# Kernel optimization log

Measured on AMD Instinct MI355X. Metric: run time of the kernel, lower is better.

Reference implementation:

```python
import jax, jax.numpy as jnp
import numpy as np

N_MQ = 50000   # number of 'mq' (user/query) nodes
N_SQ = 50000   # number of 'sq' (movie/sub-query) nodes
E = 600000     # edges of type ('mq','queries','sq'); reverse edges are the flip
EL = 200000    # supervision edges for the classifier
H = 128        # hidden_channels
F_IN = 768     # raw 'sq' feature dim (movie_lin in_features)
N_LAYERS = 4


def setup_inputs() -> dict:
    key = jax.random.key(0)
    ks = jax.random.split(key, 12)
    sH = 1.0 / np.sqrt(H)
    sF = 1.0 / np.sqrt(F_IN)
    return {
        "mq_node_id": jnp.arange(N_MQ, dtype=jnp.int64) if jax.config.jax_enable_x64 else jnp.arange(N_MQ, dtype=jnp.int32),
        "sq_node_id": jnp.arange(N_SQ, dtype=jnp.int32),
        "sq_x": jax.random.normal(ks[0], (N_SQ, F_IN), jnp.float32),
        "edge_index": jax.random.randint(ks[1], (2, E), 0, N_SQ),
        "edge_label_index": jax.random.randint(ks[2], (2, EL), 0, N_SQ),
        "user_emb": jax.random.normal(ks[3], (N_MQ, H), jnp.float32) * 0.1,
        "movie_emb": jax.random.normal(ks[4], (N_SQ, H), jnp.float32) * 0.1,
        "lin_W": jax.random.normal(ks[5], (H, F_IN), jnp.float32) * sF,
        "lin_b": jnp.zeros((H,), jnp.float32),
        "Wl_s": jax.random.normal(ks[6], (N_LAYERS, H, H), jnp.float32) * sH,
        "bl_s": jnp.zeros((N_LAYERS, H), jnp.float32),
        "Wr_s": jax.random.normal(ks[7], (N_LAYERS, H, H), jnp.float32) * sH,
        "Wl_m": jax.random.normal(ks[8], (N_LAYERS, H, H), jnp.float32) * sH,
        "bl_m": jnp.zeros((N_LAYERS, H), jnp.float32),
        "Wr_m": jax.random.normal(ks[9], (N_LAYERS, H, H), jnp.float32) * sH,
    }


def _sage(x_src, x_dst, src_idx, dst_idx, Wl, bl, Wr, n_dst):
    """PyG SAGEConv (aggr='mean', root_weight=True, bias on lin_l only)."""
    msg = x_src[src_idx]                                     # [E, H] gather
    agg = jax.ops.segment_sum(msg, dst_idx, num_segments=n_dst)
    cnt = jax.ops.segment_sum(jnp.ones((src_idx.shape[0], 1), x_src.dtype),
                              dst_idx, num_segments=n_dst)
    mean = agg / jnp.maximum(cnt, 1.0)                       # mean over in-neighbors
    return mean @ Wl.T + bl + x_dst @ Wr.T


def reference(mq_node_id, sq_node_id, sq_x, edge_index, edge_label_index,
              user_emb, movie_emb, lin_W, lin_b,
              Wl_s, bl_s, Wr_s, Wl_m, bl_m, Wr_m):
    # input encoders
    x_mq = user_emb[mq_node_id]                              # [N_MQ, H]
    x_sq = sq_x @ lin_W.T + lin_b + movie_emb[sq_node_id]    # [N_SQ, H]
    src, dst = edge_index[0], edge_index[1]                  # mq -> sq; reverse is flip
    for i in range(N_LAYERS):
        new_sq = _sage(x_mq, x_sq, src, dst, Wl_s[i], bl_s[i], Wr_s[i], N_SQ)
        new_mq = _sage(x_sq, x_mq, dst, src, Wl_m[i], bl_m[i], Wr_m[i], N_MQ)
        if i == 0:  # only conv1 has ReLU in the original GNN
            new_sq = jax.nn.relu(new_sq)
            new_mq = jax.nn.relu(new_mq)
        x_mq, x_sq = new_mq, new_sq
    # dot-product classifier over supervision edges
    return (x_mq[edge_label_index[0]] * x_sq[edge_label_index[1]]).sum(axis=-1)
```

## Files before the change

### kernel.cpp

```cpp
#include <hip/hip_runtime.h>

#define H    128
#define NMQ  50000
#define NSQ  50000
#define NE   600000
#define NEL  200000
#define FIN  768
#define NLAYERS 4

typedef __attribute__((ext_vector_type(8))) short bf16x8;
typedef __attribute__((ext_vector_type(4))) float f32x4;

__device__ inline ushort f2b(float f) {
  unsigned u = __float_as_uint(f);
  u = (u + 0x7FFFu + ((u >> 16) & 1u)) >> 16;
  return (ushort)u;
}
__device__ inline float b2f(ushort h) { return __uint_as_float((unsigned)h << 16); }

__global__ void cvt_bf16(const float* __restrict__ in, ushort* __restrict__ out, int n4) {
  int i = blockIdx.x * blockDim.x + threadIdx.x;
  if (i >= n4) return;
  float4 v = ((const float4*)in)[i];
  ushort4 o;
  o.x = f2b(v.x); o.y = f2b(v.y); o.z = f2b(v.z); o.w = f2b(v.w);
  ((ushort4*)out)[i] = o;
}

__global__ __launch_bounds__(64) void encoder_mfma(
    const float* __restrict__ A, const ushort* __restrict__ Wb,
    const float* __restrict__ bias, const float* __restrict__ memb,
    ushort* __restrict__ C)
{
  int lane = threadIdx.x;
  int rowbase = blockIdx.x * 16;
  int t = lane >> 4, fr = lane & 15;
  f32x4 acc[8];
  #pragma unroll
  for (int c = 0; c < 8; ++c)
    #pragma unroll
    for (int q = 0; q < 4; ++q) acc[c][q] = 0.f;

  int arow = rowbase + fr;
  const float* Abase = A + (long)arow * FIN + t * 8;

  for (int k0 = 0; k0 < FIN; k0 += 32) {
    bf16x8 af, bfm[8];
    {
      const float* p = Abase + k0;
      float4 v0 = *(const float4*)p;
      float4 v1 = *(const float4*)(p + 4);
      ushort tmp[8];
      tmp[0] = f2b(v0.x); tmp[1] = f2b(v0.y); tmp[2] = f2b(v0.z); tmp[3] = f2b(v0.w);
      tmp[4] = f2b(v1.x); tmp[5] = f2b(v1.y); tmp[6] = f2b(v1.z); tmp[7] = f2b(v1.w);
      af = *(bf16x8*)tmp;
    }
    #pragma unroll
    for (int cc = 0; cc < 8; ++cc) {
      int col = cc * 16 + fr;
      bfm[cc] = *(const bf16x8*)(Wb + (long)col * FIN + k0 + t * 8);
    }
    #pragma unroll
    for (int cc = 0; cc < 8; ++cc)
      acc[cc] = __builtin_amdgcn_mfma_f32_16x16x32_bf16(af, bfm[cc], acc[cc], 0, 0, 0);
  }
  #pragma unroll
  for (int cc = 0; cc < 8; ++cc)
    #pragma unroll
    for (int q = 0; q < 4; ++q) {
      int row = rowbase + t * 4 + q;
      int col = cc * 16 + fr;
      float v = acc[cc][q] + bias[col] + memb[(long)row * H + col];
      C[(long)row * H + col] = f2b(v);
    }
}

__global__ __launch_bounds__(64) void fused_layer(
    const ushort* __restrict__ xg,
    const ushort* __restrict__ xs,
    const int* __restrict__ offs, const int* __restrict__ csr,
    const ushort* __restrict__ Wl, const ushort* __restrict__ Wr,
    const float* __restrict__ bias,
    ushort* __restrict__ Cout, int M, int relu)
{
  __shared__ ushort mtile[16 * 128];
  int lane = threadIdx.x;
  int rowbase = blockIdx.x * 16;
  const unsigned* X = (const unsigned*)xg;

  int wslot = lane >> 2;
  unsigned* mt32 = (unsigned*)mtile;
  for (int i = 0; i < 16; ++i) {
    int row = rowbase + i;
    int s = offs[row], e = offs[row + 1];
    float a0 = 0.f, a1 = 0.f;
    int j = s;
    for (; j + 8 <= e; j += 8) {
      long i0 = csr[j], i1 = csr[j+1], i2 = csr[j+2], i3 = csr[j+3];
      long i4 = csr[j+4], i5 = csr[j+5], i6 = csr[j+6], i7 = csr[j+7];
      unsigned x0 = X[i0*64+lane], x1 = X[i1*64+lane], x2 = X[i2*64+lane], x3 = X[i3*64+lane];
      unsigned x4 = X[i4*64+lane], x5 = X[i5*64+lane], x6 = X[i6*64+lane], x7 = X[i7*64+lane];
      a0 += b2f((ushort)(x0 & 0xffff)) + b2f((ushort)(x1 & 0xffff))
          + b2f((ushort)(x2 & 0xffff)) + b2f((ushort)(x3 & 0xffff))
          + b2f((ushort)(x4 & 0xffff)) + b2f((ushort)(x5 & 0xffff))
          + b2f((ushort)(x6 & 0xffff)) + b2f((ushort)(x7 & 0xffff));
      a1 += b2f((ushort)(x0 >> 16)) + b2f((ushort)(x1 >> 16))
          + b2f((ushort)(x2 >> 16)) + b2f((ushort)(x3 >> 16))
          + b2f((ushort)(x4 >> 16)) + b2f((ushort)(x5 >> 16))
          + b2f((ushort)(x6 >> 16)) + b2f((ushort)(x7 >> 16));
    }
    if (j + 4 <= e) {
      long i0 = csr[j], i1 = csr[j+1], i2 = csr[j+2], i3 = csr[j+3];
      unsigned x0 = X[i0*64+lane], x1 = X[i1*64+lane], x2 = X[i2*64+lane], x3 = X[i3*64+lane];
      a0 += b2f((ushort)(x0 & 0xffff)) + b2f((ushort)(x1 & 0xffff))
          + b2f((ushort)(x2 & 0xffff)) + b2f((ushort)(x3 & 0xffff));
      a1 += b2f((ushort)(x0 >> 16)) + b2f((ushort)(x1 >> 16))
          + b2f((ushort)(x2 >> 16)) + b2f((ushort)(x3 >> 16));
      j += 4;
    }
    for (; j < e; ++j) {
      unsigned x = X[(long)csr[j] * 64 + lane];
      a0 += b2f((ushort)(x & 0xffff));
      a1 += b2f((ushort)(x >> 16));
    }
    float inv = (e > s) ? 1.f / (float)(e - s) : 0.f;
    a0 *= inv; a1 *= inv;
    int sw = (wslot & 8) | ((wslot & 7) ^ (i & 7));
    mt32[i * 64 + sw * 4 + (lane & 3)] = (unsigned)f2b(a0) | ((unsigned)f2b(a1) << 16);
  }

  int t = lane >> 4, fr = lane & 15;
  f32x4 acc[8];
  #pragma unroll
  for (int c = 0; c < 8; ++c)
    #pragma unroll
    for (int q = 0; q < 4; ++q) acc[c][q] = 0.f;

  #pragma unroll
  for (int ks = 0; ks < 4; ++ks) {
    int slot = ks * 4 + t;
    int sw = (slot & 8) | ((slot & 7) ^ (fr & 7));
    bf16x8 af = *(const bf16x8*)&mtile[fr * 128 + sw * 8];
    bf16x8 bfm[8];
    #pragma unroll
    for (int cc = 0; cc < 8; ++cc) {
      int col = cc * 16 + fr;
      bfm[cc] = *(const bf16x8*)(Wl + (long)col * H + slot * 8);
    }
    #pragma unroll
    for (int cc = 0; cc < 8; ++cc)
      acc[cc] = __builtin_amdgcn_mfma_f32_16x16x32_bf16(af, bfm[cc], acc[cc], 0, 0, 0);
  }
  int srow = rowbase + fr;
  #pragma unroll
  for (int ks = 0; ks < 4; ++ks) {
    int slot = ks * 4 + t;
    bf16x8 af = *(const bf16x8*)(xs + (long)srow * H + slot * 8);
    bf16x8 bfm[8];
    #pragma unroll
    for (int cc = 0; cc < 8; ++cc) {
      int col = cc * 16 + fr;
      bfm[cc] = *(const bf16x8*)(Wr + (long)col * H + slot * 8);
    }
    #pragma unroll
    for (int cc = 0; cc < 8; ++cc)
      acc[cc] = __builtin_amdgcn_mfma_f32_16x16x32_bf16(af, bfm[cc], acc[cc], 0, 0, 0);
  }
  #pragma unroll
  for (int cc = 0; cc < 8; ++cc)
    #pragma unroll
    for (int q = 0; q < 4; ++q) {
      int row = rowbase + t * 4 + q;
      int col = cc * 16 + fr;
      float v = acc[cc][q] + bias[col];
      if (relu) v = fmaxf(v, 0.f);
      Cout[(long)row * H + col] = f2b(v);
    }
}

__global__ void deg_count(const int* __restrict__ eidx, int* __restrict__ df, int* __restrict__ dr) {
  int e = blockIdx.x * blockDim.x + threadIdx.x;
  if (e >= NE) return;
  atomicAdd(dr + eidx[e], 1);
  atomicAdd(df + eidx[NE + e], 1);
}

__global__ __launch_bounds__(1024) void exscan2(
    const int* __restrict__ degf, const int* __restrict__ degr,
    int* __restrict__ offf, int* __restrict__ offr)
{
  __shared__ int part[1024];
  const int* deg = blockIdx.x ? degr : degf;
  int* offs = blockIdx.x ? offr : offf;
  int n = blockIdx.x ? NMQ : NSQ;
  int t = threadIdx.x;
  int chunk = (n + 1023) >> 10;
  int beg = t * chunk, end = beg + chunk;
  if (end > n) end = n;
  int s = 0;
  for (int i = beg; i < end; ++i) s += deg[i];
  part[t] = s;
  __syncthreads();
  for (int offd = 1; offd < 1024; offd <<= 1) {
    int v = 0;
    if (t >= offd) v = part[t - offd];
    __syncthreads();
    part[t] += v;
    __syncthreads();
  }
  int run = (t == 0) ? 0 : part[t - 1];
  for (int i = beg; i < end; ++i) { offs[i] = run; run += deg[i]; }
  if (t == 1023) offs[n] = part[1023];
}

__global__ void csr_fill(const int* __restrict__ eidx,
                         const int* __restrict__ offs_f, const int* __restrict__ offs_r,
                         int* __restrict__ cur_f, int* __restrict__ cur_r,
                         int* __restrict__ csr_f, int* __restrict__ csr_r) {
  int e = blockIdx.x * blockDim.x + threadIdx.x;
  if (e >= NE) return;
  int s = eidx[e], d = eidx[NE + e];
  int p = atomicAdd(cur_f + d, 1); csr_f[offs_f[d] + p] = s;
  int q = atomicAdd(cur_r + s, 1); csr_r[offs_r[s] + q] = d;
}

__global__ __launch_bounds__(256) void edge_dot_b(
    const ushort* __restrict__ xmq, const ushort* __restrict__ xsq,
    const int* __restrict__ eli, float* __restrict__ out)
{
  int wid = (blockIdx.x << 2) + (threadIdx.x >> 6);
  int lane = threadIdx.x & 63;
  if (wid >= NEL) return;
  int a = eli[wid], b = eli[NEL + wid];
  unsigned xa = ((const unsigned*)xmq)[(long)a * 64 + lane];
  unsigned xb = ((const unsigned*)xsq)[(long)b * 64 + lane];
  float p = b2f((ushort)(xa & 0xffff)) * b2f((ushort)(xb & 0xffff))
          + b2f((ushort)(xa >> 16))    * b2f((ushort)(xb >> 16));
  #pragma unroll
  for (int off = 32; off; off >>= 1) p += __shfl_down(p, off, 64);
  if (lane == 0) out[wid] = p;
}

extern "C" void kernel_launch(void* const* d_in, const int* in_sizes, int n_in,
                              void* d_out, int out_size, void* d_ws, size_t ws_size,
                              hipStream_t stream) {
  (void)in_sizes; (void)n_in; (void)out_size; (void)ws_size;
  const float* sq_x      = (const float*)d_in[2];
  const int*   eidx      = (const int*)d_in[3];
  const int*   eli       = (const int*)d_in[4];
  const float* user_emb  = (const float*)d_in[5];
  const float* movie_emb = (const float*)d_in[6];
  const float* lin_W     = (const float*)d_in[7];
  const float* lin_b     = (const float*)d_in[8];
  const float* Wl_s      = (const float*)d_in[9];
  const float* bl_s      = (const float*)d_in[10];
  const float* Wr_s      = (const float*)d_in[11];
  const float* Wl_m      = (const float*)d_in[12];
  const float* bl_m      = (const float*)d_in[13];
  const float* Wr_m      = (const float*)d_in[14];
  float* out = (float*)d_out;

  char* ws = (char*)d_ws;
  size_t off = 0;
  auto alloc = [&](size_t bytes) {
    char* p = ws + off;
    off += (bytes + 255) & ~(size_t)255;
    return p;
  };
  ushort* xmq_a = (ushort*)alloc((size_t)NMQ * H * 2);
  ushort* xmq_b = (ushort*)alloc((size_t)NMQ * H * 2);
  ushort* xsq_a = (ushort*)alloc((size_t)NSQ * H * 2);
  ushort* xsq_b = (ushort*)alloc((size_t)NSQ * H * 2);
  ushort* linWb = (ushort*)alloc((size_t)H * FIN * 2);
  ushort* Wlsb  = (ushort*)alloc((size_t)NLAYERS * H * H * 2);
  ushort* Wrsb  = (ushort*)alloc((size_t)NLAYERS * H * H * 2);
  ushort* Wlmb  = (ushort*)alloc((size_t)NLAYERS * H * H * 2);
  ushort* Wrmb  = (ushort*)alloc((size_t)NLAYERS * H * H * 2);
  int* deg_f  = (int*)alloc((size_t)NSQ * 4);
  int* deg_r  = (int*)alloc((size_t)NMQ * 4);
  int* cur_f  = (int*)alloc((size_t)NSQ * 4);
  int* cur_r  = (int*)alloc((size_t)NMQ * 4);
  int* offs_f = (int*)alloc((size_t)(NSQ + 1) * 4);
  int* offs_r = (int*)alloc((size_t)(NMQ + 1) * 4);
  int* csr_f  = (int*)alloc((size_t)NE * 4);
  int* csr_r  = (int*)alloc((size_t)NE * 4);

  hipMemsetAsync(deg_f, 0, (char*)offs_f - (char*)deg_f, stream);

  cvt_bf16<<<(NMQ * H / 4 + 255) / 256, 256, 0, stream>>>(user_emb, xmq_a, NMQ * H / 4);
  cvt_bf16<<<(H * FIN / 4 + 255) / 256, 256, 0, stream>>>(lin_W, linWb, H * FIN / 4);
  cvt_bf16<<<(NLAYERS * H * H / 4 + 255) / 256, 256, 0, stream>>>(Wl_s, Wlsb, NLAYERS * H * H / 4);
  cvt_bf16<<<(NLAYERS * H * H / 4 + 255) / 256, 256, 0, stream>>>(Wr_s, Wrsb, NLAYERS * H * H / 4);
  cvt_bf16<<<(NLAYERS * H * H / 4 + 255) / 256, 256, 0, stream>>>(Wl_m, Wlmb, NLAYERS * H * H / 4);
  cvt_bf16<<<(NLAYERS * H * H / 4 + 255) / 256, 256, 0, stream>>>(Wr_m, Wrmb, NLAYERS * H * H / 4);

  encoder_mfma<<<NSQ / 16, 64, 0, stream>>>(sq_x, linWb, lin_b, movie_emb, xsq_a);
  deg_count<<<(NE + 255) / 256, 256, 0, stream>>>(eidx, deg_f, deg_r);
  exscan2<<<2, 1024, 0, stream>>>(deg_f, deg_r, offs_f, offs_r);
  csr_fill<<<(NE + 255) / 256, 256, 0, stream>>>(eidx, offs_f, offs_r, cur_f, cur_r, csr_f, csr_r);

  ushort *cm = xmq_a, *cs = xsq_a, *nm = xmq_b, *ns = xsq_b;
  for (int l = 0; l < NLAYERS; ++l) {
    fused_layer<<<NSQ / 16, 64, 0, stream>>>(cm, cs, offs_f, csr_f,
        Wlsb + (size_t)l * H * H, Wrsb + (size_t)l * H * H, bl_s + (size_t)l * H,
        ns, NSQ, l == 0);
    fused_layer<<<NMQ / 16, 64, 0, stream>>>(cs, cm, offs_r, csr_r,
        Wlmb + (size_t)l * H * H, Wrmb + (size_t)l * H * H, bl_m + (size_t)l * H,
        nm, NMQ, l == 0);
    ushort* t;
    t = cm; cm = nm; nm = t;
    t = cs; cs = ns; ns = t;
  }
  edge_dot_b<<<(NEL + 3) / 4, 256, 0, stream>>>(cm, cs, eli, out);
}
```

Baseline: 768.3 us.

## Use two waves per block in encoder and fused layer kernels

The encoder kernel now splits the K dimension across two waves, merges the partial sums through shared memory, and prefetches the next A tile into registers. The fused layer kernel uses two waves that each gather half of the 16 rows' neighbor means, then each wave computes half of the output columns. This raises the number of waves in flight per block to hide gather and load latency, at the cost of extra block synchronisation and shared-memory traffic.

```diff
diff --git a/kernel.cpp b/kernel.cpp
--- a/kernel.cpp
+++ b/kernel.cpp
@@ -27,12 +27,13 @@
   ((ushort4*)out)[i] = o;
 }
 
-__global__ __launch_bounds__(64) void encoder_mfma(
+__global__ __launch_bounds__(128) void encoder_mfma(
     const float* __restrict__ A, const ushort* __restrict__ Wb,
     const float* __restrict__ bias, const float* __restrict__ memb,
     ushort* __restrict__ C)
 {
-  int lane = threadIdx.x;
+  __shared__ float part[16 * 128];
+  int tid = threadIdx.x, wave = tid >> 6, lane = tid & 63;
   int rowbase = blockIdx.x * 16;
   int t = lane >> 4, fr = lane & 15;
   f32x4 acc[8];
@@ -42,40 +43,58 @@
     for (int q = 0; q < 4; ++q) acc[c][q] = 0.f;
 
   int arow = rowbase + fr;
-  const float* Abase = A + (long)arow * FIN + t * 8;
-
-  for (int k0 = 0; k0 < FIN; k0 += 32) {
-    bf16x8 af, bfm[8];
-    {
-      const float* p = Abase + k0;
-      float4 v0 = *(const float4*)p;
-      float4 v1 = *(const float4*)(p + 4);
-      ushort tmp[8];
-      tmp[0] = f2b(v0.x); tmp[1] = f2b(v0.y); tmp[2] = f2b(v0.z); tmp[3] = f2b(v0.w);
-      tmp[4] = f2b(v1.x); tmp[5] = f2b(v1.y); tmp[6] = f2b(v1.z); tmp[7] = f2b(v1.w);
-      af = *(bf16x8*)tmp;
-    }
+  int kbase = wave * (FIN / 2);
+  const float* Abase = A + (long)arow * FIN + kbase + t * 8;
+  const ushort* Wbase = Wb + kbase + t * 8;
+
+  float4 p0 = *(const float4*)Abase;
+  float4 p1 = *(const float4*)(Abase + 4);
+
+  for (int ki = 0; ki < FIN / 2 / 32; ++ki) {
+    int k0 = ki * 32;
+    float4 c0 = p0, c1 = p1;
+    if (ki + 1 < FIN / 2 / 32) {
+      p0 = *(const float4*)(Abase + k0 + 32);
+      p1 = *(const float4*)(Abase + k0 + 36);
+    }
+    ushort tmp[8];
+    tmp[0] = f2b(c0.x); tmp[1] = f2b(c0.y); tmp[2] = f2b(c0.z); tmp[3] = f2b(c0.w);
+    tmp[4] = f2b(c1.x); tmp[5] = f2b(c1.y); tmp[6] = f2b(c1.z); tmp[7] = f2b(c1.w);
+    bf16x8 af = *(bf16x8*)tmp;
+    bf16x8 bfm[8];
     #pragma unroll
     for (int cc = 0; cc < 8; ++cc) {
       int col = cc * 16 + fr;
-      bfm[cc] = *(const bf16x8*)(Wb + (long)col * FIN + k0 + t * 8);
+      bfm[cc] = *(const bf16x8*)(Wbase + (long)col * FIN + k0);
     }
     #pragma unroll
     for (int cc = 0; cc < 8; ++cc)
       acc[cc] = __builtin_amdgcn_mfma_f32_16x16x32_bf16(af, bfm[cc], acc[cc], 0, 0, 0);
   }
-  #pragma unroll
-  for (int cc = 0; cc < 8; ++cc)
-    #pragma unroll
-    for (int q = 0; q < 4; ++q) {
-      int row = rowbase + t * 4 + q;
-      int col = cc * 16 + fr;
-      float v = acc[cc][q] + bias[col] + memb[(long)row * H + col];
-      C[(long)row * H + col] = f2b(v);
-    }
-}
-
-__global__ __launch_bounds__(64) void fused_layer(
+
+  if (wave == 1) {
+    #pragma unroll
+    for (int cc = 0; cc < 8; ++cc)
+      #pragma unroll
+      for (int q = 0; q < 4; ++q)
+        part[(t * 4 + q) * 128 + cc * 16 + fr] = acc[cc][q];
+  }
+  __syncthreads();
+  if (wave == 0) {
+    #pragma unroll
+    for (int cc = 0; cc < 8; ++cc)
+      #pragma unroll
+      for (int q = 0; q < 4; ++q) {
+        int row = rowbase + t * 4 + q;
+        int col = cc * 16 + fr;
+        float v = acc[cc][q] + part[(t * 4 + q) * 128 + col] + bias[col]
+                + memb[(long)row * H + col];
+        C[(long)row * H + col] = f2b(v);
+      }
+  }
+}
+
+__global__ __launch_bounds__(128) void fused_layer(
     const ushort* __restrict__ xg,
     const ushort* __restrict__ xs,
     const int* __restrict__ offs, const int* __restrict__ csr,
@@ -84,13 +103,14 @@
     ushort* __restrict__ Cout, int M, int relu)
 {
   __shared__ ushort mtile[16 * 128];
-  int lane = threadIdx.x;
+  int tid = threadIdx.x, wave = tid >> 6, lane = tid & 63;
   int rowbase = blockIdx.x * 16;
   const unsigned* X = (const unsigned*)xg;
 
   int wslot = lane >> 2;
   unsigned* mt32 = (unsigned*)mtile;
-  for (int i = 0; i < 16; ++i) {
+  for (int i8 = 0; i8 < 8; ++i8) {
+    int i = wave * 8 + i8;
     int row = rowbase + i;
     int s = offs[row], e = offs[row + 1];
     float a0 = 0.f, a1 = 0.f;
@@ -128,11 +148,12 @@
     int sw = (wslot & 8) | ((wslot & 7) ^ (i & 7));
     mt32[i * 64 + sw * 4 + (lane & 3)] = (unsigned)f2b(a0) | ((unsigned)f2b(a1) << 16);
   }
+  __syncthreads();
 
   int t = lane >> 4, fr = lane & 15;
-  f32x4 acc[8];
-  #pragma unroll
-  for (int c = 0; c < 8; ++c)
+  f32x4 acc[4];
+  #pragma unroll
+  for (int c = 0; c < 4; ++c)
     #pragma unroll
     for (int q = 0; q < 4; ++q) acc[c][q] = 0.f;
 
@@ -141,14 +162,14 @@
     int slot = ks * 4 + t;
     int sw = (slot & 8) | ((slot & 7) ^ (fr & 7));
     bf16x8 af = *(const bf16x8*)&mtile[fr * 128 + sw * 8];
-    bf16x8 bfm[8];
-    #pragma unroll
-    for (int cc = 0; cc < 8; ++cc) {
-      int col = cc * 16 + fr;
+    bf16x8 bfm[4];
+    #pragma unroll
+    for (int cc = 0; cc < 4; ++cc) {
+      int col = (wave * 4 + cc) * 16 + fr;
       bfm[cc] = *(const bf16x8*)(Wl + (long)col * H + slot * 8);
     }
     #pragma unroll
-    for (int cc = 0; cc < 8; ++cc)
+    for (int cc = 0; cc < 4; ++cc)
       acc[cc] = __builtin_amdgcn_mfma_f32_16x16x32_bf16(af, bfm[cc], acc[cc], 0, 0, 0);
   }
   int srow = rowbase + fr;
@@ -156,22 +177,22 @@
   for (int ks = 0; ks < 4; ++ks) {
     int slot = ks * 4 + t;
     bf16x8 af = *(const bf16x8*)(xs + (long)srow * H + slot * 8);
-    bf16x8 bfm[8];
-    #pragma unroll
-    for (int cc = 0; cc < 8; ++cc) {
-      int col = cc * 16 + fr;
+    bf16x8 bfm[4];
+    #pragma unroll
+    for (int cc = 0; cc < 4; ++cc) {
+      int col = (wave * 4 + cc) * 16 + fr;
       bfm[cc] = *(const bf16x8*)(Wr + (long)col * H + slot * 8);
     }
     #pragma unroll
-    for (int cc = 0; cc < 8; ++cc)
+    for (int cc = 0; cc < 4; ++cc)
       acc[cc] = __builtin_amdgcn_mfma_f32_16x16x32_bf16(af, bfm[cc], acc[cc], 0, 0, 0);
   }
   #pragma unroll
-  for (int cc = 0; cc < 8; ++cc)
+  for (int cc = 0; cc < 4; ++cc)
     #pragma unroll
     for (int q = 0; q < 4; ++q) {
       int row = rowbase + t * 4 + q;
-      int col = cc * 16 + fr;
+      int col = (wave * 4 + cc) * 16 + fr;
       float v = acc[cc][q] + bias[col];
       if (relu) v = fmaxf(v, 0.f);
       Cout[(long)row * H + col] = f2b(v);
@@ -294,17 +315,17 @@
   cvt_bf16<<<(NLAYERS * H * H / 4 + 255) / 256, 256, 0, stream>>>(Wl_m, Wlmb, NLAYERS * H * H / 4);
   cvt_bf16<<<(NLAYERS * H * H / 4 + 255) / 256, 256, 0, stream>>>(Wr_m, Wrmb, NLAYERS * H * H / 4);
 
-  encoder_mfma<<<NSQ / 16, 64, 0, stream>>>(sq_x, linWb, lin_b, movie_emb, xsq_a);
+  encoder_mfma<<<NSQ / 16, 128, 0, stream>>>(sq_x, linWb, lin_b, movie_emb, xsq_a);
   deg_count<<<(NE + 255) / 256, 256, 0, stream>>>(eidx, deg_f, deg_r);
   exscan2<<<2, 1024, 0, stream>>>(deg_f, deg_r, offs_f, offs_r);
   csr_fill<<<(NE + 255) / 256, 256, 0, stream>>>(eidx, offs_f, offs_r, cur_f, cur_r, csr_f, csr_r);
 
   ushort *cm = xmq_a, *cs = xsq_a, *nm = xmq_b, *ns = xsq_b;
   for (int l = 0; l < NLAYERS; ++l) {
-    fused_layer<<<NSQ / 16, 64, 0, stream>>>(cm, cs, offs_f, csr_f,
+    fused_layer<<<NSQ / 16, 128, 0, stream>>>(cm, cs, offs_f, csr_f,
         Wlsb + (size_t)l * H * H, Wrsb + (size_t)l * H * H, bl_s + (size_t)l * H,
         ns, NSQ, l == 0);
-    fused_layer<<<NMQ / 16, 64, 0, stream>>>(cs, cm, offs_r, csr_r,
+    fused_layer<<<NMQ / 16, 128, 0, stream>>>(cs, cm, offs_r, csr_r,
         Wlmb + (size_t)l * H * H, Wrmb + (size_t)l * H * H, bl_m + (size_t)l * H,
         nm, NMQ, l == 0);
     ushort* t;
```

After: 874.4 us. 1.14x slower.

## Gather neighbor rows into LDS via global_load_lds across whole row block

Applied to the files above, without the earlier changes.

Replaces the per-row gather loop with a flat pass over all edges of the 16-row block. Up to 64 neighbor rows per chunk are fetched straight into LDS with global_load_lds, and a per-edge destination-row array (built in csr_fill) is used to segment the means. The goal is more memory-level parallelism and less per-row loop overhead on the irregular gather. In exchange it adds a full vmcnt(0) wait per chunk, a second index array to read per edge, and 16KB of extra LDS per block, which may reduce occupancy.

```diff
diff --git a/kernel.cpp b/kernel.cpp
--- a/kernel.cpp
+++ b/kernel.cpp
@@ -7,6 +7,7 @@
 #define NEL  200000
 #define FIN  768
 #define NLAYERS 4
+#define GCHUNK 64
 
 typedef __attribute__((ext_vector_type(8))) short bf16x8;
 typedef __attribute__((ext_vector_type(4))) float f32x4;
@@ -17,6 +18,10 @@
   return (ushort)u;
 }
 __device__ inline float b2f(ushort h) { return __uint_as_float((unsigned)h << 16); }
+
+#define GLOAD_LDS(gp, lp) \
+  __builtin_amdgcn_global_load_lds((const __attribute__((address_space(1))) void*)(gp), \
+                                   (__attribute__((address_space(3))) void*)(lp), 4, 0, 0)
 
 __global__ void cvt_bf16(const float* __restrict__ in, ushort* __restrict__ out, int n4) {
   int i = blockIdx.x * blockDim.x + threadIdx.x;
@@ -79,54 +84,63 @@
     const ushort* __restrict__ xg,
     const ushort* __restrict__ xs,
     const int* __restrict__ offs, const int* __restrict__ csr,
+    const int* __restrict__ drow,
     const ushort* __restrict__ Wl, const ushort* __restrict__ Wr,
     const float* __restrict__ bias,
     ushort* __restrict__ Cout, int M, int relu)
 {
+  __shared__ unsigned stage[GCHUNK * 64];
   __shared__ ushort mtile[16 * 128];
   int lane = threadIdx.x;
   int rowbase = blockIdx.x * 16;
-  const unsigned* X = (const unsigned*)xg;
-
+  unsigned* mt32 = (unsigned*)mtile;
   int wslot = lane >> 2;
-  unsigned* mt32 = (unsigned*)mtile;
-  for (int i = 0; i < 16; ++i) {
-    int row = rowbase + i;
-    int s = offs[row], e = offs[row + 1];
-    float a0 = 0.f, a1 = 0.f;
-    int j = s;
-    for (; j + 8 <= e; j += 8) {
-      long i0 = csr[j], i1 = csr[j+1], i2 = csr[j+2], i3 = csr[j+3];
-      long i4 = csr[j+4], i5 = csr[j+5], i6 = csr[j+6], i7 = csr[j+7];
-      unsigned x0 = X[i0*64+lane], x1 = X[i1*64+lane], x2 = X[i2*64+lane], x3 = X[i3*64+lane];
-      unsigned x4 = X[i4*64+lane], x5 = X[i5*64+lane], x6 = X[i6*64+lane], x7 = X[i7*64+lane];
-      a0 += b2f((ushort)(x0 & 0xffff)) + b2f((ushort)(x1 & 0xffff))
-          + b2f((ushort)(x2 & 0xffff)) + b2f((ushort)(x3 & 0xffff))
-          + b2f((ushort)(x4 & 0xffff)) + b2f((ushort)(x5 & 0xffff))
-          + b2f((ushort)(x6 & 0xffff)) + b2f((ushort)(x7 & 0xffff));
-      a1 += b2f((ushort)(x0 >> 16)) + b2f((ushort)(x1 >> 16))
-          + b2f((ushort)(x2 >> 16)) + b2f((ushort)(x3 >> 16))
-          + b2f((ushort)(x4 >> 16)) + b2f((ushort)(x5 >> 16))
-          + b2f((ushort)(x6 >> 16)) + b2f((ushort)(x7 >> 16));
-    }
-    if (j + 4 <= e) {
-      long i0 = csr[j], i1 = csr[j+1], i2 = csr[j+2], i3 = csr[j+3];
-      unsigned x0 = X[i0*64+lane], x1 = X[i1*64+lane], x2 = X[i2*64+lane], x3 = X[i3*64+lane];
-      a0 += b2f((ushort)(x0 & 0xffff)) + b2f((ushort)(x1 & 0xffff))
-          + b2f((ushort)(x2 & 0xffff)) + b2f((ushort)(x3 & 0xffff));
-      a1 += b2f((ushort)(x0 >> 16)) + b2f((ushort)(x1 >> 16))
-          + b2f((ushort)(x2 >> 16)) + b2f((ushort)(x3 >> 16));
-      j += 4;
-    }
-    for (; j < e; ++j) {
-      unsigned x = X[(long)csr[j] * 64 + lane];
-      a0 += b2f((ushort)(x & 0xffff));
-      a1 += b2f((ushort)(x >> 16));
-    }
-    float inv = (e > s) ? 1.f / (float)(e - s) : 0.f;
-    a0 *= inv; a1 *= inv;
-    int sw = (wslot & 8) | ((wslot & 7) ^ (i & 7));
-    mt32[i * 64 + sw * 4 + (lane & 3)] = (unsigned)f2b(a0) | ((unsigned)f2b(a1) << 16);
+
+  #pragma unroll
+  for (int i = 0; i < 16; ++i) mt32[i * 64 + lane] = 0;
+
+  int cbeg = offs[rowbase], cend = offs[rowbase + 16];
+  float a0 = 0.f, a1 = 0.f;
+  int cur = -1, cnt = 0;
+
+  for (int c = cbeg; c < cend; c += GCHUNK) {
+    int n = cend - c; if (n > GCHUNK) n = GCHUNK;
+    if (n == GCHUNK) {
+      #pragma unroll
+      for (int j = 0; j < GCHUNK; ++j) {
+        long r = csr[c + j];
+        GLOAD_LDS((const char*)xg + r * 256 + lane * 4, &stage[j * 64]);
+      }
+    } else {
+      for (int j = 0; j < n; ++j) {
+        long r = csr[c + j];
+        GLOAD_LDS((const char*)xg + r * 256 + lane * 4, &stage[j * 64]);
+      }
+    }
+    asm volatile("s_waitcnt vmcnt(0)" ::: "memory");
+    __builtin_amdgcn_sched_barrier(0);
+    for (int j = 0; j < n; ++j) {
+      int rowj = drow[c + j];
+      if (rowj != cur) {
+        if (cnt > 0) {
+          float inv = 1.f / (float)cnt;
+          int sw = (wslot & 8) | ((wslot & 7) ^ (cur & 7));
+          mt32[(cur & 15) * 64 + sw * 4 + (lane & 3)] =
+              (unsigned)f2b(a0 * inv) | ((unsigned)f2b(a1 * inv) << 16);
+        }
+        cur = rowj; a0 = 0.f; a1 = 0.f; cnt = 0;
+      }
+      unsigned w = stage[j * 64 + lane];
+      a0 += b2f((ushort)(w & 0xffff));
+      a1 += b2f((ushort)(w >> 16));
+      ++cnt;
+    }
+  }
+  if (cnt > 0) {
+    float inv = 1.f / (float)cnt;
+    int sw = (wslot & 8) | ((wslot & 7) ^ (cur & 7));
+    mt32[(cur & 15) * 64 + sw * 4 + (lane & 3)] =
+        (unsigned)f2b(a0 * inv) | ((unsigned)f2b(a1 * inv) << 16);
   }
 
   int t = lane >> 4, fr = lane & 15;
@@ -216,12 +230,13 @@
 __global__ void csr_fill(const int* __restrict__ eidx,
                          const int* __restrict__ offs_f, const int* __restrict__ offs_r,
                          int* __restrict__ cur_f, int* __restrict__ cur_r,
-                         int* __restrict__ csr_f, int* __restrict__ csr_r) {
+                         int* __restrict__ csr_f, int* __restrict__ csr_r,
+                         int* __restrict__ drow_f, int* __restrict__ drow_r) {
   int e = blockIdx.x * blockDim.x + threadIdx.x;
   if (e >= NE) return;
   int s = eidx[e], d = eidx[NE + e];
-  int p = atomicAdd(cur_f + d, 1); csr_f[offs_f[d] + p] = s;
-  int q = atomicAdd(cur_r + s, 1); csr_r[offs_r[s] + q] = d;
+  int p = atomicAdd(cur_f + d, 1); int pf = offs_f[d] + p; csr_f[pf] = s; drow_f[pf] = d;
+  int q = atomicAdd(cur_r + s, 1); int pr = offs_r[s] + q; csr_r[pr] = d; drow_r[pr] = s;
 }
 
 __global__ __launch_bounds__(256) void edge_dot_b(
@@ -284,6 +299,8 @@
   int* offs_r = (int*)alloc((size_t)(NMQ + 1) * 4);
   int* csr_f  = (int*)alloc((size_t)NE * 4);
   int* csr_r  = (int*)alloc((size_t)NE * 4);
+  int* drow_f = (int*)alloc((size_t)NE * 4);
+  int* drow_r = (int*)alloc((size_t)NE * 4);
 
   hipMemsetAsync(deg_f, 0, (char*)offs_f - (char*)deg_f, stream);
 
@@ -297,14 +314,15 @@
   encoder_mfma<<<NSQ / 16, 64, 0, stream>>>(sq_x, linWb, lin_b, movie_emb, xsq_a);
   deg_count<<<(NE + 255) / 256, 256, 0, stream>>>(eidx, deg_f, deg_r);
   exscan2<<<2, 1024, 0, stream>>>(deg_f, deg_r, offs_f, offs_r);
-  csr_fill<<<(NE + 255) / 256, 256, 0, stream>>>(eidx, offs_f, offs_r, cur_f, cur_r, csr_f, csr_r);
+  csr_fill<<<(NE + 255) / 256, 256, 0, stream>>>(eidx, offs_f, offs_r, cur_f, cur_r,
+                                                 csr_f, csr_r, drow_f, drow_r);
 
   ushort *cm = xmq_a, *cs = xsq_a, *nm = xmq_b, *ns = xsq_b;
   for (int l = 0; l < NLAYERS; ++l) {
-    fused_layer<<<NSQ / 16, 64, 0, stream>>>(cm, cs, offs_f, csr_f,
+    fused_layer<<<NSQ / 16, 64, 0, stream>>>(cm, cs, offs_f, csr_f, drow_f,
         Wlsb + (size_t)l * H * H, Wrsb + (size_t)l * H * H, bl_s + (size_t)l * H,
         ns, NSQ, l == 0);
-    fused_layer<<<NMQ / 16, 64, 0, stream>>>(cs, cm, offs_r, csr_r,
+    fused_layer<<<NMQ / 16, 64, 0, stream>>>(cs, cm, offs_r, csr_r, drow_r,
         Wlmb + (size_t)l * H * H, Wrmb + (size_t)l * H * H, bl_m + (size_t)l * H,
         nm, NMQ, l == 0);
     ushort* t;
```

Result: slower. 932.2 us (+21.3%).
